# Kernel optimization log

Measured on AMD Instinct MI355X. Metric: run time of the kernel, lower is better.

## Reference

```python
import jax, jax.numpy as jnp
import numpy as np
import math

B, S, D, H = 2, 2048, 1024, 16
DH = D // H  # 64
K = 16       # relative-position clipping window (module hardcodes self.k = 16)


def setup_inputs() -> dict:
    key = jax.random.key(0)
    ks = jax.random.split(key, 16)
    p = lambda k, shape: (jax.random.normal(k, shape, dtype=jnp.float32) * 0.02)
    return {
        "query": jax.random.normal(ks[0], (B, S, D), dtype=jnp.float32),
        "key": jax.random.normal(ks[1], (B, S, D), dtype=jnp.float32),
        "value": jax.random.normal(ks[2], (B, S, D), dtype=jnp.float32),
        "q_mask": jnp.zeros((B, S), dtype=bool),
        "kv_mask": jnp.zeros((B, S), dtype=bool),
        "use_subseq_mask": 1,
        "Wq": p(ks[3], (D, D)), "bq": p(ks[4], (D,)),
        "Wk": p(ks[5], (D, D)), "bk": p(ks[6], (D,)),
        "Wv": p(ks[7], (D, D)), "bv": p(ks[8], (D,)),
        "Wo": p(ks[9], (D, D)), "bo": p(ks[10], (D,)),
        "wk_emb": p(ks[11], (2 * K + 1, DH)),
        "wv_emb": p(ks[12], (2 * K + 1, DH)),
    }


def _proj(x, W, b, pad_mask):
    # torch Linear: x @ W.T + b; then view(B,S,H,DH) -> (B,H,S,DH), zero padded positions
    h = jnp.einsum('bsd,ed->bse', x, W) + b
    h = h.reshape(x.shape[0], x.shape[1], H, DH).transpose(0, 2, 1, 3)
    return jnp.where(pad_mask[:, None, :, None], 0.0, h)


def reference(query, key, value, q_mask, kv_mask, use_subseq_mask,
              Wq, bq, Wk, bk, Wv, bv, Wo, bo, wk_emb, wv_emb):
    b = query.shape[0]
    q = _proj(query, Wq, bq, q_mask)   # [B,H,Sq,DH]
    k = _proj(key, Wk, bk, kv_mask)    # [B,H,Sk,DH]
    v = _proj(value, Wv, bv, kv_mask)  # [B,H,Sk,DH]
    Sq, Sk = q.shape[2], k.shape[2]

    # clipped relative positions: pos[i,j] = clip(j-i, -K, K) + K  (time_step=0)
    pos = jnp.clip(jnp.arange(Sk)[None, :] - jnp.arange(Sk)[:, None], -K, K) + K
    pos = pos[:Sq]  # [Sq,Sk]

    ak = wk_emb[pos]  # [Sq,Sk,DH]
    rel_score = jnp.einsum('bhqd,qvd->bhqv', q, ak)
    scores = (jnp.einsum('bhqd,bhvd->bhqv', q, k) + rel_score) / math.sqrt(DH)

    if use_subseq_mask:
        # replaces padding mask entirely, as in the original
        mask = jnp.triu(jnp.ones((Sq, Sk), dtype=bool), k=1 + Sk - Sq)[None, None]
    else:
        mask = kv_mask[:, None, None, :]
    attn = jax.nn.softmax(jnp.where(mask, -jnp.inf, scores), axis=-1)  # [B,H,Sq,Sk]

    av = wv_emb[pos]  # [Sq,Sk,DH]
    x = jnp.einsum('bhqv,bhvd->bhqd', attn, v) + jnp.einsum('bhqv,qvd->bhqd', attn, av)

    x = x.transpose(0, 2, 1, 3).reshape(b, Sq, D)
    out = jnp.einsum('bsd,ed->bse', x, Wo) + bo
    out = jnp.where(q_mask[:, :, None], 0.0, out)
    return out, attn
```

## Files before the change

kernel.cpp:

```cpp
#include <hip/hip_runtime.h>
#include <math.h>

#define BB  2
#define SS  2048
#define DD  1024
#define HH  16
#define DHH 64
#define RK  16
#define NR  33
#define BH  (BB*HH)
#define MT  (BB*SS)
#define NT  (SS/64)
#define NF  ((size_t)BH*SS*DHH)

typedef unsigned char u8;
typedef __attribute__((ext_vector_type(8))) short short8v;
typedef __attribute__((ext_vector_type(4))) float f32x4;

__device__ __forceinline__ float4 ld4(const float* p){ return *reinterpret_cast<const float4*>(p); }
__device__ __forceinline__ void st4(float* p, float4 v){ *reinterpret_cast<float4*>(p) = v; }

__device__ __forceinline__ unsigned short f2bf(float f){
    union { float f; unsigned u; } v; v.f = f;
    unsigned r = v.u + 0x7fffu + ((v.u >> 16) & 1u);
    return (unsigned short)(r >> 16);
}
__device__ __forceinline__ float bf2f(unsigned short h){
    union { unsigned u; float f; } v; v.u = ((unsigned)h) << 16;
    return v.f;
}

__device__ __forceinline__ void gemm_split_core(
    const float* __restrict__ X, const float* __restrict__ W,
    const float* __restrict__ bias, const u8* __restrict__ rmask,
    float* __restrict__ out, float scale, int qkv_mode, int m0, int n0)
{
    __shared__ short8v buf[4096];
    const int t    = threadIdx.x;
    const int lane = t & 63;
    const int w    = t >> 6;
    const int wm   = w >> 1, wn = w & 1;

    f32x4 acc[4][4];
    #pragma unroll
    for (int i=0;i<4;++i)
        #pragma unroll
        for (int j=0;j<4;++j) acc[i][j] = (f32x4){0.f,0.f,0.f,0.f};

    for (int k0 = 0; k0 < DD; k0 += 64) {
        __syncthreads();
        #pragma unroll
        for (int s = 0; s < 4; ++s) {
            const int u  = t + 256*s;
            const int ri = u >> 3, kg = u & 7;
            const int iu = (ri >> 4) & 3, ll = ri & 15;
            const int cu = kg >> 2,      lh = kg & 3;
            const int idx = (((ri >> 6)*2 + cu)*4 + iu)*64 + lh*16 + ll;
            {
                const float* gp = &X[(size_t)(m0 + ri)*DD + k0 + kg*8];
                float4 x0 = ld4(gp), x1 = ld4(gp+4);
                float xs[8] = {x0.x,x0.y,x0.z,x0.w,x1.x,x1.y,x1.z,x1.w};
                short8v h, l;
                #pragma unroll
                for (int e = 0; e < 8; ++e) {
                    unsigned short hu = f2bf(xs[e]);
                    h[e] = (short)hu;
                    l[e] = (short)f2bf(xs[e] - bf2f(hu));
                }
                buf[idx] = h; buf[1024 + idx] = l;
            }
            {
                const float* gp = &W[(size_t)(n0 + ri)*DD + k0 + kg*8];
                float4 x0 = ld4(gp), x1 = ld4(gp+4);
                float xs[8] = {x0.x,x0.y,x0.z,x0.w,x1.x,x1.y,x1.z,x1.w};
                short8v h, l;
                #pragma unroll
                for (int e = 0; e < 8; ++e) {
                    unsigned short hu = f2bf(xs[e]);
                    h[e] = (short)hu;
                    l[e] = (short)f2bf(xs[e] - bf2f(hu));
                }
                buf[2048 + idx] = h; buf[3072 + idx] = l;
            }
        }
        __syncthreads();
        #pragma unroll
        for (int c = 0; c < 2; ++c) {
            short8v ah[4], al[4], bh[4], bl[4];
            const int ab = ((wm*2 + c)*4)*64 + lane;
            const int bb = ((wn*2 + c)*4)*64 + lane;
            #pragma unroll
            for (int i = 0; i < 4; ++i) {
                ah[i] = buf[       ab + i*64];
                al[i] = buf[1024 + ab + i*64];
                bh[i] = buf[2048 + bb + i*64];
                bl[i] = buf[3072 + bb + i*64];
            }
            #pragma unroll
            for (int i = 0; i < 4; ++i)
                #pragma unroll
                for (int j = 0; j < 4; ++j) {
                    acc[i][j] = __builtin_amdgcn_mfma_f32_16x16x32_bf16(ah[i], bh[j], acc[i][j], 0,0,0);
                    acc[i][j] = __builtin_amdgcn_mfma_f32_16x16x32_bf16(ah[i], bl[j], acc[i][j], 0,0,0);
                    acc[i][j] = __builtin_amdgcn_mfma_f32_16x16x32_bf16(al[i], bh[j], acc[i][j], 0,0,0);
                }
        }
    }

    const int colb = n0 + wn*64 + (lane & 15);
    const int rowb = m0 + wm*64 + ((lane >> 4) << 2);
    #pragma unroll
    for (int j = 0; j < 4; ++j) {
        const int e  = colb + j*16;
        const float be = bias[e];
        const int hh = e >> 6, dh = e & 63;
        #pragma unroll
        for (int i = 0; i < 4; ++i) {
            #pragma unroll
            for (int r = 0; r < 4; ++r) {
                const int m = rowb + i*16 + r;
                float v = (acc[i][j][r] + be) * scale;
                if (rmask[m]) v = 0.f;
                if (qkv_mode) {
                    const int b = m >> 11, s = m & (SS-1);
                    out[(((size_t)b*HH + hh)*SS + s)*DHH + dh] = v;
                } else {
                    out[(size_t)m*DD + e] = v;
                }
            }
        }
    }
}

__global__ __launch_bounds__(256,2)
void proj_qkv_mfma(const float* __restrict__ query,
                   const float* __restrict__ key,
                   const float* __restrict__ value,
                   const float* __restrict__ Wq, const float* __restrict__ bq,
                   const float* __restrict__ Wk, const float* __restrict__ bk,
                   const float* __restrict__ Wv, const float* __restrict__ bv,
                   const u8* __restrict__ q_mask, const u8* __restrict__ kv_mask,
                   float* __restrict__ ws)
{
    const int z = blockIdx.z;
    const float* X   = (z==0)? query : (z==1)? key : value;
    const float* W   = (z==0)? Wq    : (z==1)? Wk  : Wv;
    const float* bia = (z==0)? bq    : (z==1)? bk  : bv;
    const u8* pm     = (z==0)? q_mask : kv_mask;
    float* out = ws + (size_t)z * NF;
    const float scale = (z==0)? 0.125f : 1.0f;
    gemm_split_core(X, W, bia, pm, out, scale, 1, blockIdx.y*128, blockIdx.x*128);
}

__global__ __launch_bounds__(256,2)
void proj_out_mfma(const float* __restrict__ ws,
                   const float* __restrict__ Wo, const float* __restrict__ bo,
                   const u8* __restrict__ q_mask,
                   float* __restrict__ outp)
{
    gemm_split_core(ws + 3*NF, Wo, bo, q_mask, outp, 1.0f, 0,
                    blockIdx.y*128, blockIdx.x*128);
}

__launch_bounds__(256)
__global__ void scores_kernel(const float* __restrict__ ws,
                              const float* __restrict__ wk_emb,
                              const u8* __restrict__ kv_mask,
                              const int* __restrict__ use_sub_p,
                              float* __restrict__ attn)
{
    const int qt = blockIdx.x, bh = blockIdx.y;
    const int b  = bh >> 4;
    const int use_sub = *use_sub_p;
    const int t  = threadIdx.x;
    const int tq = t>>4, tv = t&15;

    __shared__ float qs_s[DHH][68];
    __shared__ float ks_s[DHH][68];
    __shared__ float qw_s[64][NR+1];

    const float* qg = ws + ((size_t)bh*SS + (size_t)qt*64)*DHH;
    #pragma unroll
    for (int i=0;i<4;++i){
        int r = (t>>4) + 16*i;
        float4 x = ld4(&qg[(size_t)r*DHH + (t&15)*4]);
        int c = (t&15)*4;
        qs_s[c+0][r]=x.x; qs_s[c+1][r]=x.y; qs_s[c+2][r]=x.z; qs_s[c+3][r]=x.w;
    }
    float* wkf = &ks_s[0][0];
    for (int idx=t; idx < (NR*DHH)/4; idx += 256)
        ((float4*)wkf)[idx] = ((const float4*)wk_emb)[idx];
    __syncthreads();
    for (int idx=t; idx < 64*NR; idx += 256) {
        int q = idx & 63, p = idx >> 6;
        float s = 0.f;
        #pragma unroll 8
        for (int d=0; d<DHH; ++d) s = fmaf(qs_s[d][q], wkf[p*DHH+d], s);
        qw_s[q][p] = s;
    }
    __syncthreads();

    const float* kg = ws + NF + (size_t)bh*SS*DHH;
    const int vtmax = use_sub ? qt : (NT-1);
    for (int vt=0; vt<=vtmax; ++vt) {
        #pragma unroll
        for (int i=0;i<4;++i){
            int r = (t>>4) + 16*i;
            float4 x = ld4(&kg[(size_t)(vt*64+r)*DHH + (t&15)*4]);
            int c = (t&15)*4;
            ks_s[c+0][r]=x.x; ks_s[c+1][r]=x.y; ks_s[c+2][r]=x.z; ks_s[c+3][r]=x.w;
        }
        __syncthreads();
        float acc[4][4];
        #pragma unroll
        for (int i=0;i<4;++i)
            #pragma unroll
            for (int j=0;j<4;++j) acc[i][j]=0.f;
        #pragma unroll 8
        for (int kk=0; kk<DHH; ++kk) {
            float4 a4 = ld4(&qs_s[kk][tq*4]);
            float4 b4 = ld4(&ks_s[kk][tv*4]);
            float ar[4]={a4.x,a4.y,a4.z,a4.w};
            float br[4]={b4.x,b4.y,b4.z,b4.w};
            #pragma unroll
            for (int i=0;i<4;++i)
                #pragma unroll
                for (int j=0;j<4;++j) acc[i][j] = fmaf(ar[i],br[j],acc[i][j]);
        }
        #pragma unroll
        for (int i=0;i<4;++i) {
            int qi = qt*64 + tq*4 + i;
            float o[4];
            #pragma unroll
            for (int j=0;j<4;++j) {
                int vi = vt*64 + tv*4 + j;
                int d  = vi - qi;
                d = d < -RK ? -RK : (d > RK ? RK : d);
                float sc = acc[i][j] + qw_s[tq*4+i][d+RK];
                bool msk = use_sub ? (vi > qi) : (kv_mask[b*SS + vi] != 0);
                o[j] = msk ? -INFINITY : sc;
            }
            st4(&attn[((size_t)bh*SS + qi)*SS + (size_t)vt*64 + tv*4],
                make_float4(o[0],o[1],o[2],o[3]));
        }
        __syncthreads();
    }
    if (use_sub) {
        const int zc0 = (qt+1)*64;
        const float4 z4 = make_float4(0.f,0.f,0.f,0.f);
        for (int r=0; r<64; ++r) {
            float* rowp = &attn[((size_t)bh*SS + (size_t)qt*64 + r)*SS];
            for (int c = zc0 + t*4; c < SS; c += 1024) st4(&rowp[c], z4);
        }
    }
}

__launch_bounds__(256)
__global__ void rowstat_kernel(const float* __restrict__ attn,
                               const int* __restrict__ use_sub_p,
                               float* __restrict__ stats)
{
    const int use_sub = *use_sub_p;
    const int t = threadIdx.x;
    const int w = t>>6, lane = t&63;
    const int ridx = blockIdx.x*4 + w;
    const int q = ridx & (SS-1);
    const float* row = attn + (size_t)ridx * SS;
    const int vmax = use_sub ? q : (SS-1);

    float4 vals[8];
    float mx = -INFINITY;
    #pragma unroll
    for (int it=0; it<8; ++it) {
        int c = it*256 + lane*4;
        float4 x;
        if (c <= vmax) {
            x = ld4(&row[c]);
            if (c+1 > vmax) x.y = -INFINITY;
            if (c+2 > vmax) x.z = -INFINITY;
            if (c+3 > vmax) x.w = -INFINITY;
        } else { x.x=-INFINITY; x.y=-INFINITY; x.z=-INFINITY; x.w=-INFINITY; }
        vals[it] = x;
        mx = fmaxf(mx, fmaxf(fmaxf(x.x,x.y), fmaxf(x.z,x.w)));
    }
    #pragma unroll
    for (int off=1; off<64; off<<=1) mx = fmaxf(mx, __shfl_xor(mx, off));
    float sm = 0.f;
    #pragma unroll
    for (int it=0; it<8; ++it) {
        sm += expf(vals[it].x - mx) + expf(vals[it].y - mx)
            + expf(vals[it].z - mx) + expf(vals[it].w - mx);
    }
    #pragma unroll
    for (int off=1; off<64; off<<=1) sm += __shfl_xor(sm, off);
    if (lane == 0) {
        stats[(size_t)ridx*2+0] = mx;
        stats[(size_t)ridx*2+1] = 1.f/sm;
    }
}

__launch_bounds__(256)
__global__ void softmax_av_kernel(float* __restrict__ ws,
                                  const float* __restrict__ wv_emb,
                                  const int* __restrict__ use_sub_p,
                                  float* __restrict__ attn)
{
    const int qt = blockIdx.x, bh = blockIdx.y;
    const int b = bh >> 4, h = bh & 15;
    const int use_sub = *use_sub_p;
    const int t = threadIdx.x;
    const int tq = t>>4, tv = t&15;

    __shared__ float vv_s[64][68];
    __shared__ float a_s[64][68];
    __shared__ float wv_s[NR][DHH];

    const float* vg    = ws + 2*NF + (size_t)bh*SS*DHH;
    const float* stats = ws + 4*NF;
    float* xout        = ws + 3*NF;

    for (int idx=t; idx < (NR*DHH)/4; idx += 256)
        ((float4*)&wv_s[0][0])[idx] = ((const float4*)wv_emb)[idx];

    float m_i[4], invl[4];
    #pragma unroll
    for (int i=0;i<4;++i){
        size_t qi = (size_t)bh*SS + qt*64 + tq*4 + i;
        m_i[i]  = stats[qi*2+0];
        invl[i] = stats[qi*2+1];
    }
    float acc[4][4];
    #pragma unroll
    for (int i=0;i<4;++i)
        #pragma unroll
        for (int j=0;j<4;++j) acc[i][j]=0.f;
    float pb0[4]={0.f,0.f,0.f,0.f}, pb32[4]={0.f,0.f,0.f,0.f};

    const int vtmax = use_sub ? qt : (NT-1);
    for (int vt=0; vt<=vtmax; ++vt) {
        #pragma unroll
        for (int i=0;i<4;++i){
            int r = (t>>4) + 16*i;
            float4 x = ld4(&vg[(size_t)(vt*64+r)*DHH + (t&15)*4]);
            st4(&vv_s[r][(t&15)*4], x);
        }
        #pragma unroll
        for (int i=0;i<4;++i){
            int qi = qt*64 + tq*4 + i;
            float* rowp = &attn[((size_t)bh*SS + qi)*SS];
            float4 sv = ld4(&rowp[(size_t)vt*64 + tv*4]);
            float a0 = expf(sv.x - m_i[i])*invl[i];
            float a1 = expf(sv.y - m_i[i])*invl[i];
            float a2 = expf(sv.z - m_i[i])*invl[i];
            float a3 = expf(sv.w - m_i[i])*invl[i];
            st4(&rowp[(size_t)vt*64 + tv*4], make_float4(a0,a1,a2,a3));
            a_s[tv*4+0][tq*4+i]=a0; a_s[tv*4+1][tq*4+i]=a1;
            a_s[tv*4+2][tq*4+i]=a2; a_s[tv*4+3][tq*4+i]=a3;
            int v0 = vt*64 + tv*4;
            if (v0+0 <= qi-RK) pb0[i]+=a0; else if (v0+0 >= qi+RK) pb32[i]+=a0;
            if (v0+1 <= qi-RK) pb0[i]+=a1; else if (v0+1 >= qi+RK) pb32[i]+=a1;
            if (v0+2 <= qi-RK) pb0[i]+=a2; else if (v0+2 >= qi+RK) pb32[i]+=a2;
            if (v0+3 <= qi-RK) pb0[i]+=a3; else if (v0+3 >= qi+RK) pb32[i]+=a3;
        }
        __syncthreads();
        #pragma unroll 8
        for (int kk=0; kk<64; ++kk) {
            float4 a4 = ld4(&a_s[kk][tq*4]);
            float4 v4 = ld4(&vv_s[kk][tv*4]);
            float ar[4]={a4.x,a4.y,a4.z,a4.w};
            float vr[4]={v4.x,v4.y,v4.z,v4.w};
            #pragma unroll
            for (int i=0;i<4;++i)
                #pragma unroll
                for (int j=0;j<4;++j) acc[i][j] = fmaf(ar[i],vr[j],acc[i][j]);
        }
        __syncthreads();
    }

    __threadfence_block();
    __syncthreads();
    float* mid = &a_s[0][0];
    float* red = &vv_s[0][0];
    #pragma unroll
    for (int i=0;i<4;++i) red[(tq*4+i)*17 + tv] = pb0[i];
    __syncthreads();
    if (t < 64) { float s=0.f; for (int j=0;j<16;++j) s += red[t*17+j]; mid[t*34+0] = s; }
    __syncthreads();
    #pragma unroll
    for (int i=0;i<4;++i) red[(tq*4+i)*17 + tv] = pb32[i];
    __syncthreads();
    if (t < 64) {
        float s=0.f; for (int j=0;j<16;++j) s += red[t*17+j]; mid[t*34+32] = s;
        int qi = qt*64 + t;
        const float* rowp = &attn[((size_t)bh*SS + qi)*SS];
        for (int p=1; p<32; ++p) {
            int v = qi - RK + p;
            mid[t*34+p] = (v >= 0 && v < SS) ? rowp[v] : 0.f;
        }
    }
    __syncthreads();
    #pragma unroll 4
    for (int p=0; p<NR; ++p) {
        float4 w4 = ld4(&wv_s[p][tv*4]);
        #pragma unroll
        for (int i=0;i<4;++i) {
            float mm = mid[(tq*4+i)*34 + p];
            acc[i][0] = fmaf(mm,w4.x,acc[i][0]);
            acc[i][1] = fmaf(mm,w4.y,acc[i][1]);
            acc[i][2] = fmaf(mm,w4.z,acc[i][2]);
            acc[i][3] = fmaf(mm,w4.w,acc[i][3]);
        }
    }
    #pragma unroll
    for (int i=0;i<4;++i){
        int qi = qt*64 + tq*4 + i;
        st4(&xout[((size_t)b*SS + qi)*DD + h*DHH + tv*4],
            make_float4(acc[i][0],acc[i][1],acc[i][2],acc[i][3]));
    }
}

extern "C" void kernel_launch(void* const* d_in, const int* in_sizes, int n_in,
                              void* d_out, int out_size, void* d_ws, size_t ws_size,
                              hipStream_t stream)
{
    const float* query = (const float*)d_in[0];
    const float* key_  = (const float*)d_in[1];
    const float* value = (const float*)d_in[2];
    const u8*    q_mask  = (const u8*)d_in[3];
    const u8*    kv_mask = (const u8*)d_in[4];
    const int*   use_sub = (const int*)d_in[5];
    const float* Wq = (const float*)d_in[6];  const float* bq = (const float*)d_in[7];
    const float* Wk = (const float*)d_in[8];  const float* bk = (const float*)d_in[9];
    const float* Wv = (const float*)d_in[10]; const float* bv = (const float*)d_in[11];
    const float* Wo = (const float*)d_in[12]; const float* bo = (const float*)d_in[13];
    const float* wk_emb = (const float*)d_in[14];
    const float* wv_emb = (const float*)d_in[15];

    float* outp = (float*)d_out;
    float* attn = outp + (size_t)MT*DD;
    float* ws   = (float*)d_ws;
    float* stats = ws + 4*NF;

    proj_qkv_mfma<<<dim3(8,32,3), 256, 0, stream>>>(
        query, key_, value, Wq, bq, Wk, bk, Wv, bv, q_mask, kv_mask, ws);
    scores_kernel<<<dim3(NT,BH), 256, 0, stream>>>(ws, wk_emb, kv_mask, use_sub, attn);
    rowstat_kernel<<<dim3(BH*SS/4), 256, 0, stream>>>(attn, use_sub, stats);
    softmax_av_kernel<<<dim3(NT,BH), 256, 0, stream>>>(ws, wv_emb, use_sub, attn);
    proj_out_mfma<<<dim3(8,32), 256, 0, stream>>>(ws, Wo, bo, q_mask, outp);
}
```

Measured before the change: 1.532 ms.

## Fuse scores, softmax and AV into one MFMA attention kernel with split-bf16 operands

Replaces the separate scores, row-statistics and softmax-AV kernels with a single fused attention kernel. QK^T and PV now run on bf16 MFMA with hi/lo split operands, and the QKV projection writes pre-split bf16 Q/K plus a transposed V. The elided part of the diff appears to recompute row statistics inside the kernel, so the full fp32 attention matrix no longer has to be re-read between kernels. The risk is extra MFMA passes, lower precision of probabilities stored through a bf16 hi/lo pair, and occupancy changes from dropping the launch_bounds min-blocks hint.

```diff
diff --git a/kernel.cpp b/kernel.cpp
--- a/kernel.cpp
+++ b/kernel.cpp
@@ -14,26 +14,28 @@
 #define NF  ((size_t)BH*SS*DHH)
 
 typedef unsigned char u8;
+typedef unsigned short u16;
 typedef __attribute__((ext_vector_type(8))) short short8v;
 typedef __attribute__((ext_vector_type(4))) float f32x4;
 
 __device__ __forceinline__ float4 ld4(const float* p){ return *reinterpret_cast<const float4*>(p); }
 __device__ __forceinline__ void st4(float* p, float4 v){ *reinterpret_cast<float4*>(p) = v; }
 
-__device__ __forceinline__ unsigned short f2bf(float f){
+__device__ __forceinline__ u16 f2bf(float f){
     union { float f; unsigned u; } v; v.f = f;
     unsigned r = v.u + 0x7fffu + ((v.u >> 16) & 1u);
-    return (unsigned short)(r >> 16);
-}
-__device__ __forceinline__ float bf2f(unsigned short h){
+    return (u16)(r >> 16);
+}
+__device__ __forceinline__ float bf2f(u16 h){
     union { unsigned u; float f; } v; v.u = ((unsigned)h) << 16;
     return v.f;
 }
 
-__device__ __forceinline__ void gemm_split_core(
+__device__ __forceinline__ void gemm_core(
     const float* __restrict__ X, const float* __restrict__ W,
     const float* __restrict__ bias, const u8* __restrict__ rmask,
-    float* __restrict__ out, float scale, int qkv_mode, int m0, int n0)
+    float scale, int m0, int n0, int emode,
+    float* __restrict__ outf, u16* __restrict__ out_hi, u16* __restrict__ out_lo)
 {
     __shared__ short8v buf[4096];
     const int t    = threadIdx.x;
@@ -53,9 +55,9 @@
         for (int s = 0; s < 4; ++s) {
             const int u  = t + 256*s;
             const int ri = u >> 3, kg = u & 7;
-            const int iu = (ri >> 4) & 3, ll = ri & 15;
-            const int cu = kg >> 2,      lh = kg & 3;
-            const int idx = (((ri >> 6)*2 + cu)*4 + iu)*64 + lh*16 + ll;
+            const int iu = (ri >> 4) & 3, llx = ri & 15;
+            const int cu = kg >> 2,       lh = kg & 3;
+            const int idx = (((ri >> 6)*2 + cu)*4 + iu)*64 + lh*16 + llx;
             {
                 const float* gp = &X[(size_t)(m0 + ri)*DD + k0 + kg*8];
                 float4 x0 = ld4(gp), x1 = ld4(gp+4);
@@ -63,7 +65,7 @@
                 short8v h, l;
                 #pragma unroll
                 for (int e = 0; e < 8; ++e) {
-                    unsigned short hu = f2bf(xs[e]);
+                    u16 hu = f2bf(xs[e]);
                     h[e] = (short)hu;
                     l[e] = (short)f2bf(xs[e] - bf2f(hu));
                 }
@@ -76,7 +78,7 @@
                 short8v h, l;
                 #pragma unroll
                 for (int e = 0; e < 8; ++e) {
-                    unsigned short hu = f2bf(xs[e]);
+                    u16 hu = f2bf(xs[e]);
                     h[e] = (short)hu;
                     l[e] = (short)f2bf(xs[e] - bf2f(hu));
                 }
@@ -86,23 +88,23 @@
         __syncthreads();
         #pragma unroll
         for (int c = 0; c < 2; ++c) {
-            short8v ah[4], al[4], bh[4], bl[4];
+            short8v ah[4], al[4], bh2[4], bl[4];
             const int ab = ((wm*2 + c)*4)*64 + lane;
             const int bb = ((wn*2 + c)*4)*64 + lane;
             #pragma unroll
             for (int i = 0; i < 4; ++i) {
-                ah[i] = buf[       ab + i*64];
-                al[i] = buf[1024 + ab + i*64];
-                bh[i] = buf[2048 + bb + i*64];
-                bl[i] = buf[3072 + bb + i*64];
+                ah[i]  = buf[       ab + i*64];
+                al[i]  = buf[1024 + ab + i*64];
+                bh2[i] = buf[2048 + bb + i*64];
+                bl[i]  = buf[3072 + bb + i*64];
             }
             #pragma unroll
             for (int i = 0; i < 4; ++i)
                 #pragma unroll
                 for (int j = 0; j < 4; ++j) {
-                    acc[i][j] = __builtin_amdgcn_mfma_f32_16x16x32_bf16(ah[i], bh[j], acc[i][j], 0,0,0);
-                    acc[i][j] = __builtin_amdgcn_mfma_f32_16x16x32_bf16(ah[i], bl[j], acc[i][j], 0,0,0);
-                    acc[i][j] = __builtin_amdgcn_mfma_f32_16x16x32_bf16(al[i], bh[j], acc[i][j], 0,0,0);
+                    acc[i][j] = __builtin_amdgcn_mfma_f32_16x16x32_bf16(ah[i], bh2[j], acc[i][j], 0,0,0);
+                    acc[i][j] = __builtin_amdgcn_mfma_f32_16x16x32_bf16(ah[i], bl[j],  acc[i][j], 0,0,0);
+                    acc[i][j] = __builtin_amdgcn_mfma_f32_16x16x32_bf16(al[i], bh2[j], acc[i][j], 0,0,0);
                 }
         }
     }
@@ -121,18 +123,23 @@
                 const int m = rowb + i*16 + r;
                 float v = (acc[i][j][r] + be) * scale;
                 if (rmask[m]) v = 0.f;
-                if (qkv_mode) {
-                    const int b = m >> 11, s = m & (SS-1);
-                    out[(((size_t)b*HH + hh)*SS + s)*DHH + dh] = v;
+                if (emode == 0) {
+                    outf[(size_t)m*DD + e] = v;
                 } else {
-                    out[(size_t)m*DD + e] = v;
+                    u16 hb = f2bf(v);
+                    u16 lb = f2bf(v - bf2f(hb));
+                    const int b2 = m >> 11, s2 = m & (SS-1);
+                    size_t idx = (emode == 1)
+                        ? ((((size_t)b2*HH + hh)*SS + s2)*DHH + dh)
+                        : ((((size_t)b2*HH + hh)*DHH + dh)*SS + s2);
+                    out_hi[idx] = hb; out_lo[idx] = lb;
                 }
             }
         }
     }
 }
 
-__global__ __launch_bounds__(256,2)
+__global__ __launch_bounds__(256)
 void proj_qkv_mfma(const float* __restrict__ query,
                    const float* __restrict__ key,
                    const float* __restrict__ value,
@@ -140,282 +147,322 @@
                    const float* __restrict__ Wk, const float* __restrict__ bk,
                    const float* __restrict__ Wv, const float* __restrict__ bv,
                    const u8* __restrict__ q_mask, const u8* __restrict__ kv_mask,
-                   float* __restrict__ ws)
+                   u16* __restrict__ q_hi, u16* __restrict__ q_lo,
+                   u16* __restrict__ k_hi, u16* __restrict__ k_lo,
+                   u16* __restrict__ vT_hi, u16* __restrict__ vT_lo)
 {
     const int z = blockIdx.z;
     const float* X   = (z==0)? query : (z==1)? key : value;
     const float* W   = (z==0)? Wq    : (z==1)? Wk  : Wv;
     const float* bia = (z==0)? bq    : (z==1)? bk  : bv;
     const u8* pm     = (z==0)? q_mask : kv_mask;
-    float* out = ws + (size_t)z * NF;
+    u16* hi = (z==0)? q_hi : (z==1)? k_hi : vT_hi;
+    u16* lo = (z==0)? q_lo : (z==1)? k_lo : vT_lo;
     const float scale = (z==0)? 0.125f : 1.0f;
-    gemm_split_core(X, W, bia, pm, out, scale, 1, blockIdx.y*128, blockIdx.x*128);
-}
-
-__global__ __launch_bounds__(256,2)
-void proj_out_mfma(const float* __restrict__ ws,
+    const int emode = (z==2)? 2 : 1;
+    gemm_core(X, W, bia, pm, scale, blockIdx.y*128, blockIdx.x*128, emode,
+              (float*)0, hi, lo);
+}
+
+__global__ __launch_bounds__(256)
+void proj_out_mfma(const float* __restrict__ xbuf,
                    const float* __restrict__ Wo, const float* __restrict__ bo,
                    const u8* __restrict__ q_mask,
                    float* __restrict__ outp)
 {
-    gemm_split_core(ws + 3*NF, Wo, bo, q_mask, outp, 1.0f, 0,
-                    blockIdx.y*128, blockIdx.x*128);
-}
-
-__launch_bounds__(256)
-__global__ void scores_kernel(const float* __restrict__ ws,
-                              const float* __restrict__ wk_emb,
-                              const u8* __restrict__ kv_mask,
-                              const int* __restrict__ use_sub_p,
-                              float* __restrict__ attn)
-{
-    const int qt = blockIdx.x, bh = blockIdx.y;
-    const int b  = bh >> 4;
-    const int use_sub = *use_sub_p;
-    const int t  = threadIdx.x;
-    const int tq = t>>4, tv = t&15;
-
-    __shared__ float qs_s[DHH][68];
-    __shared__ float ks_s[DHH][68];
-    __shared__ float qw_s[64][NR+1];
-
-    const float* qg = ws + ((size_t)bh*SS + (size_t)qt*64)*DHH;
-    #pragma unroll
-    for (int i=0;i<4;++i){
-        int r = (t>>4) + 16*i;
-        float4 x = ld4(&qg[(size_t)r*DHH + (t&15)*4]);
-        int c = (t&15)*4;
-        qs_s[c+0][r]=x.x; qs_s[c+1][r]=x.y; qs_s[c+2][r]=x.z; qs_s[c+3][r]=x.w;
-    }
-    float* wkf = &ks_s[0][0];
-    for (int idx=t; idx < (NR*DHH)/4; idx += 256)
-        ((float4*)wkf)[idx] = ((const float4*)wk_emb)[idx];
-    __syncthreads();
-    for (int idx=t; idx < 64*NR; idx += 256) {
-        int q = idx & 63, p = idx >> 6;
-        float s = 0.f;
-        #pragma unroll 8
-        for (int d=0; d<DHH; ++d) s = fmaf(qs_s[d][q], wkf[p*DHH+d], s);
-        qw_s[q][p] = s;
-    }
-    __syncthreads();
-
-    const float* kg = ws + NF + (size_t)bh*SS*DHH;
-    const int vtmax = use_sub ? qt : (NT-1);
-    for (int vt=0; vt<=vtmax; ++vt) {
-        #pragma unroll
-        for (int i=0;i<4;++i){
-            int r = (t>>4) + 16*i;
-            float4 x = ld4(&kg[(size_t)(vt*64+r)*DHH + (t&15)*4]);
-            int c = (t&15)*4;
-            ks_s[c+0][r]=x.x; ks_s[c+1][r]=x.y; ks_s[c+2][r]=x.z; ks_s[c+3][r]=x.w;
-        }
-        __syncthreads();
-        float acc[4][4];
-        #pragma unroll
-        for (int i=0;i<4;++i)
-            #pragma unroll
-            for (int j=0;j<4;++j) acc[i][j]=0.f;
-        #pragma unroll 8
-        for (int kk=0; kk<DHH; ++kk) {
-            float4 a4 = ld4(&qs_s[kk][tq*4]);
-            float4 b4 = ld4(&ks_s[kk][tv*4]);
-            float ar[4]={a4.x,a4.y,a4.z,a4.w};
-            float br[4]={b4.x,b4.y,b4.z,b4.w};
-            #pragma unroll
-            for (int i=0;i<4;++i)
-                #pragma unroll
-                for (int j=0;j<4;++j) acc[i][j] = fmaf(ar[i],br[j],acc[i][j]);
-        }
-        #pragma unroll
-        for (int i=0;i<4;++i) {
-            int qi = qt*64 + tq*4 + i;
-            float o[4];
-            #pragma unroll
-            for (int j=0;j<4;++j) {
-                int vi = vt*64 + tv*4 + j;
-                int d  = vi - qi;
-                d = d < -RK ? -RK : (d > RK ? RK : d);
-                float sc = acc[i][j] + qw_s[tq*4+i][d+RK];
-                bool msk = use_sub ? (vi > qi) : (kv_mask[b*SS + vi] != 0);
-                o[j] = msk ? -INFINITY : sc;
-            }
-            st4(&attn[((size_t)bh*SS + qi)*SS + (size_t)vt*64 + tv*4],
-                make_float4(o[0],o[1],o[2],o[3]));
-        }
-        __syncthreads();
-    }
-    if (use_sub) {
-        const int zc0 = (qt+1)*64;
-        const float4 z4 = make_float4(0.f,0.f,0.f,0.f);
-        for (int r=0; r<64; ++r) {
-            float* rowp = &attn[((size_t)bh*SS + (size_t)qt*64 + r)*SS];
-            for (int c = zc0 + t*4; c < SS; c += 1024) st4(&rowp[c], z4);
-        }
-    }
-}
-
-__launch_bounds__(256)
-__global__ void rowstat_kernel(const float* __restrict__ attn,
-                               const int* __restrict__ use_sub_p,
-                               float* __restrict__ stats)
-{
-    const int use_sub = *use_sub_p;
-    const int t = threadIdx.x;
-    const int w = t>>6, lane = t&63;
-    const int ridx = blockIdx.x*4 + w;
-    const int q = ridx & (SS-1);
-    const float* row = attn + (size_t)ridx * SS;
-    const int vmax = use_sub ? q : (SS-1);
-
-    float4 vals[8];
-    float mx = -INFINITY;
-    #pragma unroll
-    for (int it=0; it<8; ++it) {
-        int c = it*256 + lane*4;
-        float4 x;
-        if (c <= vmax) {
-            x = ld4(&row[c]);
-            if (c+1 > vmax) x.y = -INFINITY;
-            if (c+2 > vmax) x.z = -INFINITY;
-            if (c+3 > vmax) x.w = -INFINITY;
-        } else { x.x=-INFINITY; x.y=-INFINITY; x.z=-INFINITY; x.w=-INFINITY; }
-        vals[it] = x;
-        mx = fmaxf(mx, fmaxf(fmaxf(x.x,x.y), fmaxf(x.z,x.w)));
-    }
-    #pragma unroll
-    for (int off=1; off<64; off<<=1) mx = fmaxf(mx, __shfl_xor(mx, off));
-    float sm = 0.f;
-    #pragma unroll
-    for (int it=0; it<8; ++it) {
-        sm += expf(vals[it].x - mx) + expf(vals[it].y - mx)
-            + expf(vals[it].z - mx) + expf(vals[it].w - mx);
-    }
-    #pragma unroll
-    for (int off=1; off<64; off<<=1) sm += __shfl_xor(sm, off);
-    if (lane == 0) {
-        stats[(size_t)ridx*2+0] = mx;
-        stats[(size_t)ridx*2+1] = 1.f/sm;
-    }
-}
-
-__launch_bounds__(256)
-__global__ void softmax_av_kernel(float* __restrict__ ws,
-                                  const float* __restrict__ wv_emb,
-                                  const int* __restrict__ use_sub_p,
-                                  float* __restrict__ attn)
+    gemm_core(xbuf, Wo, bo, q_mask, 1.0f, blockIdx.y*128, blockIdx.x*128, 0,
+              outp, (u16*)0, (u16*)0);
+}
+
+__global__ __launch_bounds__(256)
+void attn_fused(const u16* __restrict__ q_hi, const u16* __restrict__ q_lo,
+                const u16* __restrict__ k_hi, const u16* __restrict__ k_lo,
+                const u16* __restrict__ vT_hi, const u16* __restrict__ vT_lo,
+                const float* __restrict__ wk_emb, const float* __restrict__ wv_emb,
+                const u8* __restrict__ kv_mask, const int* __restrict__ use_sub_p,
+                float* __restrict__ attn, float* __restrict__ xbuf)
 {
     const int qt = blockIdx.x, bh = blockIdx.y;
     const int b = bh >> 4, h = bh & 15;
     const int use_sub = *use_sub_p;
     const int t = threadIdx.x;
-    const int tq = t>>4, tv = t&15;
-
-    __shared__ float vv_s[64][68];
-    __shared__ float a_s[64][68];
+    const int lane = t & 63, w = t >> 6;
+    const int lg = lane >> 4, ll = lane & 15;
+
+    __shared__ __align__(16) u16 Pbuf[2][64][72];
+    __shared__ float qw_s[64][36];
     __shared__ float wv_s[NR][DHH];
-
-    const float* vg    = ws + 2*NF + (size_t)bh*SS*DHH;
-    const float* stats = ws + 4*NF;
-    float* xout        = ws + 3*NF;
-
-    for (int idx=t; idx < (NR*DHH)/4; idx += 256)
+    __shared__ float red_s[4][64][2];
+    __shared__ float mid_s[64][36];
+    __shared__ float stat_s[64][2];
+
+    const int q0 = qt*64;
+    const size_t qrow0 = (size_t)bh*SS + q0;
+    float* attn_base = attn + ((size_t)bh*SS + q0)*SS;
+
+    for (int idx = t; idx < 64*8; idx += 256) {
+        int r = idx >> 3, c8 = idx & 7;
+        *(short8v*)&Pbuf[0][r][c8*8] = *(const short8v*)&q_hi[(qrow0 + r)*DHH + c8*8];
+        *(short8v*)&Pbuf[1][r][c8*8] = *(const short8v*)&q_lo[(qrow0 + r)*DHH + c8*8];
+    }
+    float* wkf = &mid_s[0][0];
+    for (int idx = t; idx < (NR*DHH)/4; idx += 256)
+        ((float4*)wkf)[idx] = ((const float4*)wk_emb)[idx];
+    for (int idx = t; idx < (NR*DHH)/4; idx += 256)
         ((float4*)&wv_s[0][0])[idx] = ((const float4*)wv_emb)[idx];
-
-    float m_i[4], invl[4];
-    #pragma unroll
-    for (int i=0;i<4;++i){
-        size_t qi = (size_t)bh*SS + qt*64 + tq*4 + i;
-        m_i[i]  = stats[qi*2+0];
-        invl[i] = stats[qi*2+1];
-    }
-    float acc[4][4];
+    __syncthreads();
+
+    for (int idx = t; idx < 64*NR; idx += 256) {
+        int q = idx & 63, p = idx >> 6;
+        float s = 0.f;
+        #pragma unroll 8
+        for (int d = 0; d < DHH; ++d) {
+            float qv = bf2f(Pbuf[0][q][d]) + bf2f(Pbuf[1][q][d]);
+            s = fmaf(qv, wkf[p*DHH + d], s);
+        }
+        qw_s[q][p] = s;
+    }
+    short8v qa_h[4][2], qa_l[4][2];
+    #pragma unroll
+    for (int i = 0; i < 4; ++i)
+        #pragma unroll
+        for (int c = 0; c < 2; ++c) {
+            qa_h[i][c] = *(short8v*)&Pbuf[0][16*i + ll][c*32 + lg*8];
+            qa_l[i][c] = *(short8v*)&Pbuf[1][16*i + ll][c*32 + lg*8];
+        }
+    __syncthreads();
+
+    const int vtmax = use_sub ? qt : (NT-1);
+    const int vcol  = 16*w + ll;
+
+    if (use_sub) {
+        const float4 z4 = make_float4(0.f,0.f,0.f,0.f);
+        const int row = t >> 2, cg = (t & 3)*16;
+        for (int vt = qt+1; vt < NT; ++vt) {
+            float* tb = attn_base + vt*64;
+            #pragma unroll
+            for (int u2 = 0; u2 < 4; ++u2)
+                st4(tb + (size_t)row*SS + cg + u2*4, z4);
+        }
+    }
+
+    float rm[4][4], rl[4][4];
     #pragma unroll
     for (int i=0;i<4;++i)
         #pragma unroll
-        for (int j=0;j<4;++j) acc[i][j]=0.f;
-    float pb0[4]={0.f,0.f,0.f,0.f}, pb32[4]={0.f,0.f,0.f,0.f};
-
-    const int vtmax = use_sub ? qt : (NT-1);
-    for (int vt=0; vt<=vtmax; ++vt) {
-        #pragma unroll
-        for (int i=0;i<4;++i){
-            int r = (t>>4) + 16*i;
-            float4 x = ld4(&vg[(size_t)(vt*64+r)*DHH + (t&15)*4]);
-            st4(&vv_s[r][(t&15)*4], x);
-        }
-        #pragma unroll
-        for (int i=0;i<4;++i){
-            int qi = qt*64 + tq*4 + i;
-            float* rowp = &attn[((size_t)bh*SS + qi)*SS];
-            float4 sv = ld4(&rowp[(size_t)vt*64 + tv*4]);
-            float a0 = expf(sv.x - m_i[i])*invl[i];
-            float a1 = expf(sv.y - m_i[i])*invl[i];
-            float a2 = expf(sv.z - m_i[i])*invl[i];
-            float a3 = expf(sv.w - m_i[i])*invl[i];
-            st4(&rowp[(size_t)vt*64 + tv*4], make_float4(a0,a1,a2,a3));
-            a_s[tv*4+0][tq*4+i]=a0; a_s[tv*4+1][tq*4+i]=a1;
-            a_s[tv*4+2][tq*4+i]=a2; a_s[tv*4+3][tq*4+i]=a3;
-            int v0 = vt*64 + tv*4;
-            if (v0+0 <= qi-RK) pb0[i]+=a0; else if (v0+0 >= qi+RK) pb32[i]+=a0;
-            if (v0+1 <= qi-RK) pb0[i]+=a1; else if (v0+1 >= qi+RK) pb32[i]+=a1;
-            if (v0+2 <= qi-RK) pb0[i]+=a2; else if (v0+2 >= qi+RK) pb32[i]+=a2;
-            if (v0+3 <= qi-RK) pb0[i]+=a3; else if (v0+3 >= qi+RK) pb32[i]+=a3;
-        }
+        for (int r=0;r<4;++r){ rm[i][r]=-INFINITY; rl[i][r]=0.f; }
+
+    for (int vt = 0; vt <= vtmax; ++vt) {
+        const size_t vrow = (size_t)bh*SS + vt*64 + vcol;
+        short8v kb_h[2], kb_l[2];
+        #pragma unroll
+        for (int c=0;c<2;++c){
+            kb_h[c] = *(const short8v*)&k_hi[vrow*DHH + c*32 + lg*8];
+            kb_l[c] = *(const short8v*)&k_lo[vrow*DHH + c*32 + lg*8];
+        }
+        f32x4 acc[4];
+        #pragma unroll
+        for (int i=0;i<4;++i) acc[i]=(f32x4){0.f,0.f,0.f,0.f};
+        #pragma unroll
+        for (int c=0;c<2;++c)
+            #pragma unroll
+            for (int i=0;i<4;++i){
+                acc[i] = __builtin_amdgcn_mfma_f32_16x16x32_bf16(qa_h[i][c], kb_h[c], acc[i],0,0,0);
+                acc[i] = __builtin_amdgcn_mfma_f32_16x16x32_bf16(qa_h[i][c], kb_l[c], acc[i],0,0,0);
+                acc[i] = __builtin_amdgcn_mfma_f32_16x16x32_bf16(qa_l[i][c], kb_h[c], acc[i],0,0,0);
+            }
+        const int vglob = vt*64 + vcol;
+        const bool colmask = (!use_sub) && (kv_mask[b*SS + vglob] != 0);
+        #pragma unroll
+        for (int i=0;i<4;++i)
+            #pragma unroll
+            for (int r=0;r<4;++r){
+                const int qloc = 16*i + 4*lg + r;
+                const int qglob = q0 + qloc;
+                int d = vglob - qglob; d = d<-RK?-RK:(d>RK?RK:d);
+                float s = acc[i][r] + qw_s[qloc][d+RK];
+                const bool msk = use_sub ? (vglob > qglob) : colmask;
+                if (msk) s = -INFINITY;
+                float mn = fmaxf(rm[i][r], s);
+                if (mn > -INFINITY) {
+                    rl[i][r] = rl[i][r]*__expf(rm[i][r]-mn) + __expf(s-mn);
+                    rm[i][r] = mn;
+                }
+            }
+    }
+    #pragma unroll
+    for (int i=0;i<4;++i)
+        #pragma unroll
+        for (int r=0;r<4;++r){
+            float m = rm[i][r], l = rl[i][r];
+            #pragma unroll
+            for (int off=1; off<16; off<<=1){
+                float om = __shfl_xor(m, off);
+                float ol = __shfl_xor(l, off);
+                float mn = fmaxf(m, om);
+                float e1 = (m  > -INFINITY)? __expf(m  - mn) : 0.f;
+                float e2 = (om > -INFINITY)? __expf(om - mn) : 0.f;
+                l = l*e1 + ol*e2; m = mn;
+            }
+            if (ll == 0) { const int qloc = 16*i + 4*lg + r;
+                red_s[w][qloc][0] = m; red_s[w][qloc][1] = l; }
+        }
+    __syncthreads();
+    if (t < 64) {
+        float m = red_s[0][t][0], l = red_s[0][t][1];
+        #pragma unroll
+        for (int w2=1; w2<4; ++w2){
+            float om = red_s[w2][t][0], ol = red_s[w2][t][1];
+            float mn = fmaxf(m, om);
+            float e1 = (m >-INFINITY)? __expf(m -mn) : 0.f;
+            float e2 = (om>-INFINITY)? __expf(om-mn) : 0.f;
+            l = l*e1 + ol*e2; m = mn;
+        }
+        stat_s[t][0] = m; stat_s[t][1] = 1.f/l;
+    }
+    __syncthreads();
+
+    float pb0[4][4], pb32[4][4];
+    #pragma unroll
+    for (int i=0;i<4;++i)
+        #pragma unroll
+        for (int r=0;r<4;++r){ pb0[i][r]=0.f; pb32[i][r]=0.f; }
+    f32x4 xac[4];
+    #pragma unroll
+    for (int i=0;i<4;++i) xac[i]=(f32x4){0.f,0.f,0.f,0.f};
+
+    for (int vt = 0; vt <= vtmax; ++vt) {
+        const size_t vrow = (size_t)bh*SS + vt*64 + vcol;
+        short8v kb_h[2], kb_l[2];
+        #pragma unroll
+        for (int c=0;c<2;++c){
+            kb_h[c] = *(const short8v*)&k_hi[vrow*DHH + c*32 + lg*8];
+            kb_l[c] = *(const short8v*)&k_lo[vrow*DHH + c*32 + lg*8];
+        }
+        f32x4 acc[4];
+        #pragma unroll
+        for (int i=0;i<4;++i) acc[i]=(f32x4){0.f,0.f,0.f,0.f};
+        #pragma unroll
+        for (int c=0;c<2;++c)
+            #pragma unroll
+            for (int i=0;i<4;++i){
+                acc[i] = __builtin_amdgcn_mfma_f32_16x16x32_bf16(qa_h[i][c], kb_h[c], acc[i],0,0,0);
+                acc[i] = __builtin_amdgcn_mfma_f32_16x16x32_bf16(qa_h[i][c], kb_l[c], acc[i],0,0,0);
+                acc[i] = __builtin_amdgcn_mfma_f32_16x16x32_bf16(qa_l[i][c], kb_h[c], acc[i],0,0,0);
+            }
+        const int vglob = vt*64 + vcol;
+        const bool colmask = (!use_sub) && (kv_mask[b*SS + vglob] != 0);
+
         __syncthreads();
-        #pragma unroll 8
-        for (int kk=0; kk<64; ++kk) {
-            float4 a4 = ld4(&a_s[kk][tq*4]);
-            float4 v4 = ld4(&vv_s[kk][tv*4]);
-            float ar[4]={a4.x,a4.y,a4.z,a4.w};
-            float vr[4]={v4.x,v4.y,v4.z,v4.w};
-            #pragma unroll
-            for (int i=0;i<4;++i)
+        #pragma unroll
+        for (int i=0;i<4;++i)
+            #pragma unroll
+            for (int r=0;r<4;++r){
+                const int qloc = 16*i + 4*lg + r;
+                const int qglob = q0 + qloc;
+                int d = vglob - qglob; d = d<-RK?-RK:(d>RK?RK:d);
+                float s = acc[i][r] + qw_s[qloc][d+RK];
+                const bool msk = use_sub ? (vglob > qglob) : colmask;
+                float p = msk ? 0.f : __expf(s - stat_s[qloc][0]) * stat_s[qloc][1];
+                u16 hb = f2bf(p);
+                Pbuf[0][qloc][vcol] = hb;
+                Pbuf[1][qloc][vcol] = f2bf(p - bf2f(hb));
+                if (vglob <= qglob - RK)      pb0[i][r]  += p;
+                else if (vglob >= qglob + RK) pb32[i][r] += p;
+            }
+        __syncthreads();
+
+        {
+            float* tb = attn_base + vt*64;
+            const int row = t >> 2, cg = (t & 3)*16;
+            #pragma unroll
+            for (int u2=0; u2<4; ++u2){
+                const int c0 = cg + u2*4;
+                float4 o;
+                o.x = bf2f(Pbuf[0][row][c0+0]) + bf2f(Pbuf[1][row][c0+0]);
+                o.y = bf2f(Pbuf[0][row][c0+1]) + bf2f(Pbuf[1][row][c0+1]);
+                o.z = bf2f(Pbuf[0][row][c0+2]) + bf2f(Pbuf[1][row][c0+2]);
+                o.w = bf2f(Pbuf[0][row][c0+3]) + bf2f(Pbuf[1][row][c0+3]);
+                st4(tb + (size_t)row*SS + c0, o);
+            }
+        }
+        {
+            const size_t dvrow = ((size_t)bh*DHH + 16*w + ll)*SS + (size_t)vt*64;
+            short8v vb_h[2], vb_l[2];
+            #pragma unroll
+            for (int c=0;c<2;++c){
+                vb_h[c] = *(const short8v*)&vT_hi[dvrow + c*32 + lg*8];
+                vb_l[c] = *(const short8v*)&vT_lo[dvrow + c*32 + lg*8];
+            }
+            #pragma unroll
+            for (int i=0;i<4;++i){
                 #pragma unroll
-                for (int j=0;j<4;++j) acc[i][j] = fmaf(ar[i],vr[j],acc[i][j]);
-        }
-        __syncthreads();
-    }
-
+                for (int c=0;c<2;++c){
+                    short8v pa_h = *(short8v*)&Pbuf[0][16*i + ll][c*32 + lg*8];
+                    short8v pa_l = *(short8v*)&Pbuf[1][16*i + ll][c*32 + lg*8];
+                    xac[i] = __builtin_amdgcn_mfma_f32_16x16x32_bf16(pa_h, vb_h[c], xac[i],0,0,0);
+                    xac[i] = __builtin_amdgcn_mfma_f32_16x16x32_bf16(pa_h, vb_l[c], xac[i],0,0,0);
+                    xac[i] = __builtin_amdgcn_mfma_f32_16x16x32_bf16(pa_l, vb_h[c], xac[i],0,0,0);
+                }
+            }
+        }
+    }
+
+    #pragma unroll
+    for (int i=0;i<4;++i)
+        #pragma unroll
+        for (int r=0;r<4;++r){
+            float a0 = pb0[i][r], a2 = pb32[i][r];
+            #pragma unroll
+            for (int off=1; off<16; off<<=1){
+                a0 += __shfl_xor(a0, off);
+                a2 += __shfl_xor(a2, off);
+            }
+            if (ll == 0){ const int qloc = 16*i + 4*lg + r;
+                red_s[w][qloc][0] = a0; red_s[w][qloc][1] = a2; }
+        }
     __threadfence_block();
     __syncthreads();
-    float* mid = &a_s[0][0];
-    float* red = &vv_s[0][0];
-    #pragma unroll
-    for (int i=0;i<4;++i) red[(tq*4+i)*17 + tv] = pb0[i];
+    if (t < 64) {
+        mid_s[t][0]  = red_s[0][t][0]+red_s[1][t][0]+red_s[2][t][0]+red_s[3][t][0];
+        mid_s[t][32] = red_s[0][t][1]+red_s[1][t][1]+red_s[2][t][1]+red_s[3][t][1];
+        const int qglob = q0 + t;
+        const float* rowp = attn_base + (size_t)t*SS;
+        #pragma unroll 4
+        for (int p=1; p<32; ++p){
+            const int v = qglob - RK + p;
+            mid_s[t][p] = (v >= 0 && v < SS) ? rowp[v] : 0.f;
+        }
+    }
+    float* xs = reinterpret_cast<float*>(&Pbuf[0][0][0]);
+    #pragma unroll
+    for (int i=0;i<4;++i)
+        #pragma unroll
+        for (int r=0;r<4;++r)
+            xs[(16*i + 4*lg + r)*66 + 16*w + ll] = xac[i][r];
     __syncthreads();
-    if (t < 64) { float s=0.f; for (int j=0;j<16;++j) s += red[t*17+j]; mid[t*34+0] = s; }
-    __syncthreads();
-    #pragma unroll
-    for (int i=0;i<4;++i) red[(tq*4+i)*17 + tv] = pb32[i];
-    __syncthreads();
-    if (t < 64) {
-        float s=0.f; for (int j=0;j<16;++j) s += red[t*17+j]; mid[t*34+32] = s;
-        int qi = qt*64 + t;
-        const float* rowp = &attn[((size_t)bh*SS + qi)*SS];
-        for (int p=1; p<32; ++p) {
-            int v = qi - RK + p;
-            mid[t*34+p] = (v >= 0 && v < SS) ? rowp[v] : 0.f;
-        }
-    }
-    __syncthreads();
-    #pragma unroll 4
-    for (int p=0; p<NR; ++p) {
-        float4 w4 = ld4(&wv_s[p][tv*4]);
-        #pragma unroll
-        for (int i=0;i<4;++i) {
-            float mm = mid[(tq*4+i)*34 + p];
-            acc[i][0] = fmaf(mm,w4.x,acc[i][0]);
-            acc[i][1] = fmaf(mm,w4.y,acc[i][1]);
-            acc[i][2] = fmaf(mm,w4.z,acc[i][2]);
-            acc[i][3] = fmaf(mm,w4.w,acc[i][3]);
-        }
-    }
-    #pragma unroll
-    for (int i=0;i<4;++i){
-        int qi = qt*64 + tq*4 + i;
-        st4(&xout[((size_t)b*SS + qi)*DD + h*DHH + tv*4],
-            make_float4(acc[i][0],acc[i][1],acc[i][2],acc[i][3]));
+
+    {
+        const int row = t >> 2, dg = (t & 3)*16;
+        float av[16];
+        #pragma unroll
+        for (int e=0;e<16;++e) av[e] = xs[row*66 + dg + e];
+        #pragma unroll 4
+        for (int p=0; p<NR; ++p){
+            const float mm = mid_s[row][p];
+            #pragma unroll
+            for (int u2=0; u2<4; ++u2){
+                float4 w4 = ld4(&wv_s[p][dg + u2*4]);
+                av[u2*4+0] = fmaf(mm, w4.x, av[u2*4+0]);
+                av[u2*4+1] = fmaf(mm, w4.y, av[u2*4+1]);
+                av[u2*4+2] = fmaf(mm, w4.z, av[u2*4+2]);
+                av[u2*4+3] = fmaf(mm, w4.w, av[u2*4+3]);
+            }
+        }
+        float* xg = xbuf + ((size_t)(b*SS + q0 + row))*DD + h*DHH + dg;
+        #pragma unroll
+        for (int u2=0; u2<4; ++u2)
+            st4(xg + u2*4, make_float4(av[u2*4+0],av[u2*4+1],av[u2*4+2],av[u2*4+3]));
     }
 }
 
@@ -438,13 +485,18 @@
 
     float* outp = (float*)d_out;
     float* attn = outp + (size_t)MT*DD;
-    float* ws   = (float*)d_ws;
-    float* stats = ws + 4*NF;
+
+    u16* wsu   = (u16*)d_ws;
+    u16* q_hi  = wsu;          u16* q_lo  = wsu + NF;
+    u16* k_hi  = wsu + 2*NF;   u16* k_lo  = wsu + 3*NF;
+    u16* vT_hi = wsu + 4*NF;   u16* vT_lo = wsu + 5*NF;
+    float* xbuf = (float*)(wsu + 6*NF);
 
     proj_qkv_mfma<<<dim3(8,32,3), 256, 0, stream>>>(
-        query, key_, value, Wq, bq, Wk, bk, Wv, bv, q_mask, kv_mask, ws);
-    scores_kernel<<<dim3(NT,BH), 256, 0, stream>>>(ws, wk_emb, kv_mask, use_sub, attn);
-    rowstat_kernel<<<dim3(BH*SS/4), 256, 0, stream>>>(attn, use_sub, stats);
-    softmax_av_kernel<<<dim3(NT,BH), 256, 0, stream>>>(ws, wv_emb, use_sub, attn);
-    proj_out_mfma<<<dim3(8,32), 256, 0, stream>>>(ws, Wo, bo, q_mask, outp);
-}
+        query, key_, value, Wq, bq, Wk, bk, Wv, bv, q_mask, kv_mask,
+        q_hi, q_lo, k_hi, k_lo, vT_hi, vT_lo);
+    attn_fused<<<dim3(NT,BH), 256, 0, stream>>>(
+        q_hi, q_lo, k_hi, k_lo, vT_hi, vT_lo,
+        wk_emb, wv_emb, kv_mask, use_sub, attn, xbuf);
+    proj_out_mfma<<<dim3(8,32), 256, 0, stream>>>(xbuf, Wo, bo, q_mask, outp);
+}
```

Result: faster. 1.419 ms (-7.3%).
